# Kernel optimization log

Measured on AMD Instinct MI355X. Metric: run time of the kernel, lower is better.

## Reference

```python
import jax, jax.numpy as jnp
import numpy as np

D_MODEL = 1024
D_STATE = 128
D_CONV = 4
EXPAND = 2
HEADDIM = 64
NGROUPS = 1
CHUNK = 256
D_INNER = EXPAND * D_MODEL          # 2048
NHEADS = D_INNER // HEADDIM         # 32
D_IN_PROJ = 2 * D_INNER + 2 * NGROUPS * D_STATE + NHEADS  # 4384
CONV_DIM = D_INNER + 2 * NGROUPS * D_STATE                # 2304
BATCH, SEQLEN = 2, 2048


def rmsnorm(x, w, eps=1e-6):
    ms = jnp.mean(x * x, axis=-1, keepdims=True)
    return w * (x * jax.lax.rsqrt(ms + eps))


def layernorm(x, eps=1e-5):
    mu = jnp.mean(x, axis=-1, keepdims=True)
    var = jnp.mean((x - mu) ** 2, axis=-1, keepdims=True)
    return (x - mu) * jax.lax.rsqrt(var + eps)


def activation_quant(x):
    # int8-style fake quant with STE, scale differentiable (matches torch)
    amax = jnp.clip(jnp.max(jnp.abs(x), axis=-1, keepdims=True), 1e-5, None)
    scale = 127.0 / amax
    q = jnp.clip(jnp.round(x * scale), -128, 127)
    return (jax.lax.stop_gradient(q - x * scale) + x * scale) / scale


def weight_quant(w):
    # ternary {-1,0,1}; note: NOT rescaled by scale (matches the triton kernel)
    scale = jnp.clip(jnp.mean(jnp.abs(w)), 1e-5, None)
    wq = jnp.clip(jnp.round(w / scale), -1.0, 1.0)
    return w + jax.lax.stop_gradient(wq - w)  # STE: identity grad


def bitlinear(x, w):
    return activation_quant(layernorm(x)) @ weight_quant(w).T


def segsum(x):
    # x: [..., T] -> [..., T, T] lower-triangular cumulative segment sums
    T = x.shape[-1]
    cs = jnp.cumsum(x, axis=-1)
    ss = cs[..., :, None] - cs[..., None, :]
    mask = jnp.tril(jnp.ones((T, T), dtype=bool))
    return jnp.where(mask, ss, -jnp.inf)


def ssd(u, a, B, C, chunk):
    # u: b l h p (= x*dt); a: b l h (= A*dt); B, C: b l h n (per-head)
    b, l, h, p = u.shape
    n = B.shape[-1]
    c = l // chunk
    u = u.reshape(b, c, chunk, h, p)
    a = a.reshape(b, c, chunk, h).transpose(0, 3, 1, 2)   # b h c s
    B = B.reshape(b, c, chunk, h, n)
    C = C.reshape(b, c, chunk, h, n)
    a_cs = jnp.cumsum(a, axis=-1)                          # b h c s
    L = jnp.exp(segsum(a))                                 # b h c s s
    Y_diag = jnp.einsum('bclhn,bcshn,bhcls,bcshp->bclhp', C, B, L, u)
    decay_states = jnp.exp(a_cs[..., -1:] - a_cs)          # b h c s
    states = jnp.einsum('bclhn,bhcl,bclhp->bchpn', B, decay_states, u)
    a_chunk = jnp.pad(a_cs[..., -1], ((0, 0), (0, 0), (1, 0)))  # b h (c+1)
    decay_chunk = jnp.exp(segsum(a_chunk))                 # b h (c+1) (c+1)
    states = jnp.concatenate([jnp.zeros_like(states[:, :1]), states], axis=1)
    new_states = jnp.einsum('bhzc,bchpn->bzhpn', decay_chunk, states)
    prev_states = new_states[:, :-1]                       # state entering each chunk
    Y_off = jnp.einsum('bclhn,bchpn,bhcl->bclhp', C, prev_states, jnp.exp(a_cs))
    return (Y_diag + Y_off).reshape(b, l, h, p)


def setup_inputs() -> dict:
    key = jax.random.key(0)
    ks = jax.random.split(key, 6)
    hidden_states = jax.random.normal(ks[0], (BATCH, SEQLEN, D_MODEL), jnp.float32)
    in_proj_w = jax.random.normal(ks[1], (D_IN_PROJ, D_MODEL), jnp.float32) / np.sqrt(D_MODEL).astype(np.float32)
    out_proj_w = jax.random.normal(ks[2], (D_MODEL, D_INNER), jnp.float32) / np.sqrt(D_INNER).astype(np.float32)
    conv_w = jax.random.normal(ks[3], (CONV_DIM, D_CONV), jnp.float32) * 0.1
    conv_b = jnp.zeros((CONV_DIM,), jnp.float32)
    A_log = jnp.log(jnp.arange(1, NHEADS + 1, dtype=jnp.float32))
    Dp = jnp.ones((NHEADS,), jnp.float32)
    dt_min, dt_max, dt_floor = 1e-3, 1e-1, 1e-4
    inv_dt = jnp.exp(jax.random.uniform(ks[4], (NHEADS,)) * (np.log(dt_max) - np.log(dt_min)) + np.log(dt_min))
    inv_dt = jnp.clip(inv_dt, dt_floor, None)
    dt_bias = inv_dt + jnp.log(-jnp.expm1(-inv_dt))
    norm_w = jnp.ones((D_MODEL,), jnp.float32)
    out_norm_w = jnp.ones((D_INNER,), jnp.float32)
    return dict(hidden_states=hidden_states, norm_w=norm_w, in_proj_w=in_proj_w,
                conv_w=conv_w, conv_b=conv_b, A_log=A_log, Dp=Dp, dt_bias=dt_bias,
                out_norm_w=out_norm_w, out_proj_w=out_proj_w)


def reference(hidden_states, norm_w, in_proj_w, conv_w, conv_b, A_log, Dp, dt_bias, out_norm_w, out_proj_w):
    b, l, _ = hidden_states.shape
    h = rmsnorm(hidden_states, norm_w)
    zxbcdt = bitlinear(h, in_proj_w)                       # b l (2*d_inner + 2*g*n + h)
    z = zxbcdt[..., :D_INNER]
    xBC = zxbcdt[..., D_INNER:D_INNER + CONV_DIM]
    dt = zxbcdt[..., D_INNER + CONV_DIM:]                  # b l h
    # causal depthwise conv1d (kernel D_CONV) + silu
    xp = jnp.pad(xBC, ((0, 0), (D_CONV - 1, 0), (0, 0)))
    conv = sum(xp[:, k:k + l, :] * conv_w[:, k] for k in range(D_CONV)) + conv_b
    xBC = jax.nn.silu(conv)
    x = xBC[..., :D_INNER].reshape(b, l, NHEADS, HEADDIM)
    Bm = xBC[..., D_INNER:D_INNER + NGROUPS * D_STATE].reshape(b, l, NGROUPS, D_STATE)
    Cm = xBC[..., D_INNER + NGROUPS * D_STATE:].reshape(b, l, NGROUPS, D_STATE)
    hpg = NHEADS // NGROUPS
    Bh = jnp.repeat(Bm, hpg, axis=2)                       # b l h n
    Ch = jnp.repeat(Cm, hpg, axis=2)
    dt = jax.nn.softplus(dt + dt_bias)                     # dt_softplus=True
    A = -jnp.exp(A_log)
    y = ssd(x * dt[..., None], dt * A, Bh, Ch, CHUNK)      # b l h p
    y = y + x * Dp[None, None, :, None]                    # D skip
    y = y * jax.nn.silu(z).reshape(b, l, NHEADS, HEADDIM)  # z gate
    y = rmsnorm(y.reshape(b, l, D_INNER), out_norm_w)
    out = bitlinear(y, out_proj_w)
    return hidden_states + out
```

## Files before the change

### kernel.cpp

```cpp
#include <hip/hip_runtime.h>
#include <stdint.h>
#include <stddef.h>
#include <math.h>

#define TOKS 4096
#define DM   1024
#define DIP  4384
#define DI   2048
#define CVD  2304
#define NH   32
#define HD   64
#define DST  128
#define NCH  8
#define CHK  256

typedef int v4i  __attribute__((ext_vector_type(4)));
typedef int v16i __attribute__((ext_vector_type(16)));
typedef short s8v __attribute__((ext_vector_type(8)));
typedef float f16v __attribute__((ext_vector_type(16)));
typedef unsigned short ushort_t;

static const size_t OFF_ZX    = 0;
static const size_t OFF_SX    = OFF_ZX + (size_t)TOKS*DIP*4;
static const size_t OFF_ST    = OFF_SX + (size_t)TOKS*CVD*4;
static const size_t OFF_YG    = OFF_ST + (size_t)512*HD*DST*4;
static const size_t OFF_Q1    = OFF_YG + (size_t)TOKS*DI*4;
static const size_t OFF_Q2    = OFF_Q1 + (size_t)TOKS*DM;
static const size_t OFF_WQ1   = OFF_Q2 + (size_t)TOKS*DI;
static const size_t OFF_WQ2   = OFF_WQ1 + (size_t)DIP*DM;
static const size_t OFF_RS1   = OFF_WQ2 + (size_t)DM*DI;
static const size_t OFF_RS2   = OFF_RS1 + (size_t)TOKS*4;
static const size_t OFF_DT    = OFF_RS2 + (size_t)TOKS*4;
static const size_t OFF_ACS   = OFF_DT + (size_t)TOKS*NH*4;
static const size_t OFF_CSUM  = OFF_ACS + (size_t)512*CHK*8;
static const size_t OFF_PART  = OFF_CSUM + 512*8;
static const size_t OFF_WSC   = OFF_PART + 1024*8;
static const size_t OFF_BH    = OFF_WSC + 64;
static const size_t OFF_BL    = OFF_BH  + (size_t)TOKS*128*2;
static const size_t OFF_CHG   = OFF_BL  + (size_t)TOKS*128*2;
static const size_t OFF_CLG   = OFF_CHG + (size_t)TOKS*128*2;
static const size_t OFF_GRAM  = OFF_CLG + (size_t)TOKS*128*2;
static const size_t OFF_UTH   = OFF_GRAM + (size_t)16*256*256*4;
static const size_t OFF_UTL   = OFF_UTH + (size_t)512*64*256*2;
static const size_t OFF_PH    = OFF_UTL + (size_t)512*64*256*2;
static const size_t OFF_PL    = OFF_PH  + (size_t)512*64*128*2;

__device__ __forceinline__ ushort_t f2bf(float x) {
  union { float f; unsigned int u; } v; v.f = x;
  unsigned int r = v.u + 0x7FFFu + ((v.u >> 16) & 1u);
  return (ushort_t)(r >> 16);
}
__device__ __forceinline__ float bf2f(ushort_t h) {
  union { unsigned int u; float f; } v; v.u = ((unsigned int)h) << 16;
  return v.f;
}

__device__ __forceinline__ double bsumd(double v, double* sb) {
#pragma unroll
  for (int o = 32; o; o >>= 1) v += __shfl_down(v, o);
  int lane = threadIdx.x & 63, w = threadIdx.x >> 6;
  __syncthreads();
  if (lane == 0) sb[w] = v;
  __syncthreads();
  return sb[0] + sb[1] + sb[2] + sb[3];
}
__device__ __forceinline__ double bmaxd(double v, double* sb) {
#pragma unroll
  for (int o = 32; o; o >>= 1) v = fmax(v, __shfl_down(v, o));
  int lane = threadIdx.x & 63, w = threadIdx.x >> 6;
  __syncthreads();
  if (lane == 0) sb[w] = v;
  __syncthreads();
  return fmax(fmax(sb[0], sb[1]), fmax(sb[2], sb[3]));
}

__global__ void __launch_bounds__(256) k_absmean(const float* __restrict__ w, int n, double* __restrict__ part) {
  double s = 0.0;
  for (int i = blockIdx.x * 256 + threadIdx.x; i < n; i += 512 * 256) s += (double)fabsf(w[i]);
  __shared__ double sb[4];
  s = bsumd(s, sb);
  if (threadIdx.x == 0) part[blockIdx.x] = s;
}

__global__ void __launch_bounds__(256) k_wscale(const double* __restrict__ part, double* __restrict__ wsc, int n1, int n2) {
  __shared__ double sb[4];
  double s = part[threadIdx.x] + part[threadIdx.x + 256];
  double t1 = bsumd(s, sb);
  __syncthreads();
  s = part[512 + threadIdx.x] + part[512 + threadIdx.x + 256];
  double t2 = bsumd(s, sb);
  if (threadIdx.x == 0) {
    wsc[0] = fmax(t1 / (double)n1, 1e-5);
    wsc[1] = fmax(t2 / (double)n2, 1e-5);
  }
}

__global__ void __launch_bounds__(256) k_tern(const float* __restrict__ w, int n, const double* __restrict__ wsc, int which, int8_t* __restrict__ out) {
  int i = blockIdx.x * 256 + threadIdx.x;
  if (i < n) {
    double sc = wsc[which];
    double q = fmin(fmax(rint((double)w[i] / sc), -1.0), 1.0);
    out[i] = (int8_t)q;
  }
}

template <int D>
__global__ void __launch_bounds__(256) k_normquant(const float* __restrict__ in, const float* __restrict__ w,
                                                   int8_t* __restrict__ q, float* __restrict__ rs) {
  constexpr int E = D / 256;
  int t = blockIdx.x, tid = threadIdx.x;
  const float* row = in + (size_t)t * D;
  __shared__ double sb[4];
  double x[E];
  double ss = 0.0;
#pragma unroll
  for (int i = 0; i < E; i++) { x[i] = (double)row[tid + 256 * i]; ss += x[i] * x[i]; }
  ss = bsumd(ss, sb);
  double rr = 1.0 / sqrt(ss / (double)D + 1e-6);
  double s1 = 0.0;
#pragma unroll
  for (int i = 0; i < E; i++) { x[i] = (double)w[tid + 256 * i] * (x[i] * rr); s1 += x[i]; }
  s1 = bsumd(s1, sb);
  double mu = s1 / (double)D;
  double s2 = 0.0;
#pragma unroll
  for (int i = 0; i < E; i++) { double d = x[i] - mu; s2 += d * d; }
  s2 = bsumd(s2, sb);
  double rv = 1.0 / sqrt(s2 / (double)D + 1e-5);
  double am = 0.0;
#pragma unroll
  for (int i = 0; i < E; i++) { x[i] = (x[i] - mu) * rv; am = fmax(am, fabs(x[i])); }
  am = bmaxd(am, sb);
  am = fmax(am, 1e-5);
  double sc = 127.0 / am;
#pragma unroll
  for (int i = 0; i < E; i++) {
    double qq = fmin(fmax(rint(x[i] * sc), -128.0), 127.0);
    q[(size_t)t * D + tid + 256 * i] = (int8_t)qq;
  }
  if (tid == 0) rs[t] = (float)(am / 127.0);
}

__global__ void __launch_bounds__(256, 3) k_gemm_mfma(const int8_t* __restrict__ A, const int8_t* __restrict__ W,
                                                      const float* __restrict__ rs, const float* __restrict__ addend,
                                                      float* __restrict__ out, int M, int N, int K) {
  __shared__ int8_t Al[128 * 80];
  __shared__ int8_t Bl[128 * 80];
  int m0 = blockIdx.x * 128, n0 = blockIdx.y * 128;
  int t = threadIdx.x;
  int w = t >> 6, lane = t & 63;
  int wm = w >> 1, wn = w & 1;
  int l31 = lane & 31, lh = lane >> 5;

  v16i acc[2][2] = {};

  for (int k0 = 0; k0 < K; k0 += 64) {
    __syncthreads();
#pragma unroll
    for (int it = 0; it < 2; ++it) {
      int c = t + 256 * it;
      int row = c >> 2, kc = (c & 3) * 16;
      int4 av = *(const int4*)(A + (size_t)(m0 + row) * K + k0 + kc);
      *(int4*)(Al + row * 80 + kc) = av;
      int4 bv;
      if (n0 + row < N) bv = *(const int4*)(W + (size_t)(n0 + row) * K + k0 + kc);
      else { bv.x = bv.y = bv.z = bv.w = 0; }
      *(int4*)(Bl + row * 80 + kc) = bv;
    }
    __syncthreads();
#pragma unroll
    for (int ks = 0; ks < 2; ++ks) {
      v4i af[2], bf[2];
#pragma unroll
      for (int tm = 0; tm < 2; ++tm)
        af[tm] = *(const v4i*)(Al + (wm * 64 + tm * 32 + l31) * 80 + ks * 32 + lh * 16);
#pragma unroll
      for (int tn = 0; tn < 2; ++tn)
        bf[tn] = *(const v4i*)(Bl + (wn * 64 + tn * 32 + l31) * 80 + ks * 32 + lh * 16);
#pragma unroll
      for (int tm = 0; tm < 2; ++tm)
#pragma unroll
        for (int tn = 0; tn < 2; ++tn)
          acc[tm][tn] = __builtin_amdgcn_mfma_i32_32x32x32_i8(af[tm], bf[tn], acc[tm][tn], 0, 0, 0);
    }
  }

#pragma unroll
  for (int tm = 0; tm < 2; ++tm)
#pragma unroll
    for (int tn = 0; tn < 2; ++tn) {
      int n = n0 + wn * 64 + tn * 32 + l31;
      if (n < N) {
#pragma unroll
        for (int r = 0; r < 16; ++r) {
          int mrel = (r & 3) + 8 * (r >> 2) + 4 * lh;
          int m = m0 + wm * 64 + tm * 32 + mrel;
          float v = rs[m] * (float)acc[tm][tn][r];
          if (addend) v += addend[(size_t)m * N + n];
          out[(size_t)m * N + n] = v;
        }
      }
    }
}

__global__ void __launch_bounds__(256) k_conv(const float* __restrict__ zx, const float* __restrict__ cw,
                                              const float* __restrict__ cb, float* __restrict__ sx) {
  int c = blockIdx.x * 256 + threadIdx.x;
  int t = blockIdx.y;
  int b = t >> 11, l = t & 2047;
  float acc = cb[c];
#pragma unroll
  for (int k = 0; k < 4; k++) {
    int li = l - 3 + k;
    if (li >= 0) acc = fmaf(zx[(size_t)(b * 2048 + li) * DIP + DI + c], cw[c * 4 + k], acc);
  }
  sx[(size_t)t * CVD + c] = acc / (1.f + expf(-acc));
}

__global__ void __launch_bounds__(256) k_splitbc(const float* __restrict__ sx,
                                                 ushort_t* __restrict__ bh, ushort_t* __restrict__ bl,
                                                 ushort_t* __restrict__ ch, ushort_t* __restrict__ cl) {
  int idx = blockIdx.x * 256 + threadIdx.x;
  int tok = idx >> 6, c4 = (idx & 63) * 4;
  float4 v = *(const float4*)(sx + (size_t)tok * CVD + DI + c4);
  float f[4] = {v.x, v.y, v.z, v.w};
  ushort_t hh[4], ll[4];
#pragma unroll
  for (int j = 0; j < 4; j++) { hh[j] = f2bf(f[j]); ll[j] = f2bf(f[j] - bf2f(hh[j])); }
  uint2 hv, lv;
  hv.x = (unsigned)hh[0] | ((unsigned)hh[1] << 16); hv.y = (unsigned)hh[2] | ((unsigned)hh[3] << 16);
  lv.x = (unsigned)ll[0] | ((unsigned)ll[1] << 16); lv.y = (unsigned)ll[2] | ((unsigned)ll[3] << 16);
  if (c4 < 128) {
    *(uint2*)(bh + (size_t)tok * 128 + c4) = hv;
    *(uint2*)(bl + (size_t)tok * 128 + c4) = lv;
  } else {
    *(uint2*)(ch + (size_t)tok * 128 + c4 - 128) = hv;
    *(uint2*)(cl + (size_t)tok * 128 + c4 - 128) = lv;
  }
}

__global__ void __launch_bounds__(256) k_dt(const float* __restrict__ zx, const float* __restrict__ dt_bias,
                                            float* __restrict__ dtv) {
  int idx = blockIdx.x * 256 + threadIdx.x;
  int t = idx >> 5, h = idx & 31;
  float x = zx[(size_t)t * DIP + (DI + CVD) + h] + dt_bias[h];
  dtv[idx] = fmaxf(x, 0.f) + log1pf(expf(-fabsf(x)));
}

__global__ void __launch_bounds__(256) k_cumsum(const float* __restrict__ dtv, const float* __restrict__ A_log,
                                                double* __restrict__ acs, double* __restrict__ csum) {
  int bid = blockIdx.x;
  int h = bid & 31, bc = bid >> 5;
  int s = threadIdx.x;
  int tok = bc * 256 + s;
  double negA = -exp((double)A_log[h]);
  double a = (double)dtv[tok * 32 + h] * negA;
  __shared__ double buf[256];
  buf[s] = a;
  __syncthreads();
  for (int o = 1; o < 256; o <<= 1) {
    double add = (s >= o) ? buf[s - o] : 0.0;
    __syncthreads();
    buf[s] += add;
    __syncthreads();
  }
  acs[(size_t)bid * 256 + s] = buf[s];
  if (s == 255) csum[bid] = buf[s];
}

__global__ void __launch_bounds__(256) k_gram(const ushort_t* __restrict__ bhg, const ushort_t* __restrict__ blg,
                                              const ushort_t* __restrict__ chg, const ushort_t* __restrict__ clg,
                                              float* __restrict__ gram) {
  int blk = blockIdx.x;
  int bc = blk >> 3, lt = blk & 7;
  int t = threadIdx.x;
  int w = t >> 6, lane = t & 63;
  int l31 = lane & 31, lhf = lane >> 5;
  __shared__ float Gl[4][32 * 36];

  s8v ch[8], cl[8];
  size_t tokA = (size_t)(bc * 256 + lt * 32 + l31) * 128;
#pragma unroll
  for (int ks = 0; ks < 8; ++ks) {
    ch[ks] = *(const s8v*)(chg + tokA + ks * 16 + lhf * 8);
    cl[ks] = *(const s8v*)(clg + tokA + ks * 16 + lhf * 8);
  }
  for (int st = w; st <= lt; st += 4) {
    size_t tokB = (size_t)(bc * 256 + st * 32 + l31) * 128;
    f16v acc = {};
#pragma unroll
    for (int ks = 0; ks < 8; ++ks) {
      s8v bh = *(const s8v*)(bhg + tokB + ks * 16 + lhf * 8);
      s8v bl = *(const s8v*)(blg + tokB + ks * 16 + lhf * 8);
      acc = __builtin_amdgcn_mfma_f32_32x32x16_bf16(ch[ks], bh, acc, 0, 0, 0);
      acc = __builtin_amdgcn_mfma_f32_32x32x16_bf16(ch[ks], bl, acc, 0, 0, 0);
      acc = __builtin_amdgcn_mfma_f32_32x32x16_bf16(cl[ks], bh, acc, 0, 0, 0);
    }
#pragma unroll
    for (int rr = 0; rr < 16; ++rr) {
      int lrow = (rr & 3) + 8 * (rr >> 2) + 4 * lhf;
      Gl[w][lrow * 36 + l31] = acc[rr];
    }
    int lr = lane >> 1, c0 = (lane & 1) * 16;
    float* gdst = gram + ((size_t)bc * 256 + lt * 32 + lr) * 256 + st * 32 + c0;
#pragma unroll
    for (int i = 0; i < 4; ++i)
      *(float4*)(gdst + i * 4) = *(const float4*)(&Gl[w][lr * 36 + c0 + i * 4]);
  }
}

__global__ void __launch_bounds__(256) k_prepuT(const float* __restrict__ sx, const float* __restrict__ dtv,
                                                ushort_t* __restrict__ uth, ushort_t* __restrict__ utl) {
  int r = blockIdx.x;
  int h = r & 31, bc = r >> 5;
  int t = threadIdx.x;
  __shared__ float Xs[64 * 68];
  __shared__ float dts[64];
  for (int slab = 0; slab < 4; ++slab) {
    int s0 = slab * 64;
    if (slab) __syncthreads();
    if (t < 64) dts[t] = dtv[(size_t)(bc * 256 + s0 + t) * 32 + h];
    {
      int s = t >> 2, pg = (t & 3) * 16;
      const float* xr = sx + (size_t)(bc * 256 + s0 + s) * CVD + h * 64 + pg;
      float* dst = &Xs[s * 68 + pg];
#pragma unroll
      for (int i = 0; i < 4; ++i)
        *(float4*)(dst + i * 4) = *(const float4*)(xr + i * 4);
    }
    __syncthreads();
    {
      int p = t >> 2, sg = (t & 3) * 16;
      union { int4 q[2]; ushort_t e[16]; } H, L;
#pragma unroll
      for (int j = 0; j < 16; ++j) {
        float f = Xs[(sg + j) * 68 + p] * dts[sg + j];
        ushort_t hh = f2bf(f);
        H.e[j] = hh;
        L.e[j] = f2bf(f - bf2f(hh));
      }
      size_t base = ((size_t)r * 64 + p) * 256 + s0 + sg;
      *(int4*)(uth + base) = H.q[0];
      *(int4*)(uth + base + 8) = H.q[1];
      *(int4*)(utl + base) = L.q[0];
      *(int4*)(utl + base + 8) = L.q[1];
    }
  }
}

__global__ void __launch_bounds__(256, 4) k_states2(const float* __restrict__ sx, const float* __restrict__ dtv,
                                                    const double* __restrict__ acs, const double* __restrict__ csum,
                                                    float* __restrict__ states) {
  int r = blockIdx.x;
  int h = r & 31, bc = r >> 5;
  int t = threadIdx.x, tx = t & 15, ty = t >> 4;
  __shared__ float du[64 * 68];
  double last = csum[r];
  float acc[4][8] = {};
  for (int s0 = 0; s0 < 256; s0 += 64) {
    __syncthreads();
    {
      int s = t >> 2, pg = (t & 3) * 16;
      int tok = bc * 256 + s0 + s;
      float w = expf((float)(last - acs[(size_t)r * 256 + s0 + s])) * dtv[(size_t)tok * 32 + h];
      const float* xr = sx + (size_t)tok * CVD + h * 64 + pg;
      float* dst = &du[s * 68 + pg];
#pragma unroll
      for (int i = 0; i < 4; i++) {
        float4 v = *(const float4*)(xr + i * 4);
        v.x *= w; v.y *= w; v.z *= w; v.w *= w;
        *(float4*)(dst + i * 4) = v;
      }
    }
    __syncthreads();
#pragma unroll 4
    for (int s = 0; s < 64; s++) {
      int tok = bc * 256 + s0 + s;
      const float* br = sx + (size_t)tok * CVD + DI + ty * 8;
      float4 b0 = *(const float4*)(br);
      float4 b1 = *(const float4*)(br + 4);
      float4 d4 = *(const float4*)(&du[s * 68 + tx * 4]);
      float dd[4] = {d4.x, d4.y, d4.z, d4.w};
      float bv[8] = {b0.x, b0.y, b0.z, b0.w, b1.x, b1.y, b1.z, b1.w};
#pragma unroll
      for (int i = 0; i < 4; i++)
#pragma unroll
        for (int j = 0; j < 8; j++) acc[i][j] = fmaf(dd[i], bv[j], acc[i][j]);
    }
  }
  size_t base = (size_t)r * (HD * DST);
#pragma unroll
  for (int i = 0; i < 4; i++) {
    float4 v0, v1;
    v0.x = acc[i][0]; v0.y = acc[i][1]; v0.z = acc[i][2]; v0.w = acc[i][3];
    v1.x = acc[i][4]; v1.y = acc[i][5]; v1.z = acc[i][6]; v1.w = acc[i][7];
    *(float4*)(states + base + (size_t)(tx * 4 + i) * DST + ty * 8) = v0;
    *(float4*)(states + base + (size_t)(tx * 4 + i) * DST + ty * 8 + 4) = v1;
  }
}

__global__ void __launch_bounds__(256) k_chunkscan(float* __restrict__ states, const double* __restrict__ csum,
                                                   ushort_t* __restrict__ ph, ushort_t* __restrict__ pl) {
  int idx = blockIdx.x * 256 + threadIdx.x;
  int n = idx & 127, p = (idx >> 7) & 63, h = (idx >> 13) & 31, b = idx >> 18;
  float Nv = 0.f;
  for (int c = 0; c < 8; c++) {
    int bid = (b * 8 + c) * 32 + h;
    size_t addr = (size_t)bid * (HD * DST) + p * DST + n;
    float s = states[addr];
    states[addr] = Nv;
    ushort_t hh = f2bf(Nv);
    ph[addr] = hh;
    pl[addr] = f2bf(Nv - bf2f(hh));
    Nv = Nv * expf((float)csum[bid]) + s;
  }
}

__global__ void __launch_bounds__(64) k_y7(const float* __restrict__ sx, const double* __restrict__ acs,
                                           const ushort_t* __restrict__ chg, const ushort_t* __restrict__ clg,
                                           const ushort_t* __restrict__ prevh, const ushort_t* __restrict__ prevl,
                                           const float* __restrict__ gram,
                                           const ushort_t* __restrict__ uth, const ushort_t* __restrict__ utl,
                                           const float* __restrict__ zx, const float* __restrict__ Dp,
                                           float* __restrict__ yg) {
  int myid = (blockIdx.x & 7) * 512 + (blockIdx.x >> 3);
  int r = myid >> 3, lt = myid & 7;
  int h = r & 31, bc = r >> 5;
  int lane = threadIdx.x;
  int l31 = lane & 31, lhf = lane >> 5;
  int lw = lt * 32;
  int lg = lw + l31;
  const double* acsr = acs + (size_t)r * 256;
  double a_l = acsr[lg];

  f16v Yacc[2] = {};
  {
    size_t ca = (size_t)(bc * 256 + lg) * 128;
#pragma unroll
    for (int ks = 0; ks < 8; ++ks) {
      s8v ch = *(const s8v*)(chg + ca + ks * 16 + lhf * 8);
      s8v cl = *(const s8v*)(clg + ca + ks * 16 + lhf * 8);
#pragma unroll
      for (int pt = 0; pt < 2; ++pt) {
        size_t pa = ((size_t)r * 64 + pt * 32 + l31) * 128 + ks * 16 + lhf * 8;
        s8v ph = *(const s8v*)(prevh + pa);
        s8v pl = *(const s8v*)(prevl + pa);
        Yacc[pt] = __builtin_amdgcn_mfma_f32_32x32x16_bf16(ch, ph, Yacc[pt], 0, 0, 0);
        Yacc[pt] = __builtin_amdgcn_mfma_f32_32x32x16_bf16(ch, pl, Yacc[pt], 0, 0, 0);
        Yacc[pt] = __builtin_amdgcn_mfma_f32_32x32x16_bf16(cl, ph, Yacc[pt], 0, 0, 0);
      }
    }
  }
#pragma unroll
  for (int rr = 0; rr < 16; ++rr) {
    int lrow = (rr & 3) + 8 * (rr >> 2) + 4 * lhf;
    float el = expf((float)acsr[lw + lrow]);
    Yacc[0][rr] *= el;
    Yacc[1][rr] *= el;
  }

  for (int st = 0; st <= lt; ++st) {
    int s0 = st * 32;
    const float* gp = gram + (size_t)(bc * 256 + lg) * 256 + s0;
#pragma unroll
    for (int ks2 = 0; ks2 < 2; ++ks2) {
      int kb = ks2 * 16 + lhf * 8;
      float4 g0 = *(const float4*)(gp + kb);
      float4 g1 = *(const float4*)(gp + kb + 4);
      float gv[8] = {g0.x, g0.y, g0.z, g0.w, g1.x, g1.y, g1.z, g1.w};
      union { s8v v; ushort_t e[8]; } AH, AL;
#pragma unroll
      for (int j = 0; j < 8; ++j) {
        int s = s0 + kb + j;
        float v = 0.f;
        if (s <= lg) v = expf((float)(a_l - acsr[s])) * gv[j];
        ushort_t hh = f2bf(v);
        AH.e[j] = hh;
        AL.e[j] = f2bf(v - bf2f(hh));
      }
#pragma unroll
      for (int pt = 0; pt < 2; ++pt) {
        size_t ub = ((size_t)r * 64 + pt * 32 + l31) * 256 + s0 + kb;
        s8v uh = *(const s8v*)(uth + ub);
        s8v ul = *(const s8v*)(utl + ub);
        Yacc[pt] = __builtin_amdgcn_mfma_f32_32x32x16_bf16(AH.v, uh, Yacc[pt], 0, 0, 0);
        Yacc[pt] = __builtin_amdgcn_mfma_f32_32x32x16_bf16(AH.v, ul, Yacc[pt], 0, 0, 0);
        Yacc[pt] = __builtin_amdgcn_mfma_f32_32x32x16_bf16(AL.v, uh, Yacc[pt], 0, 0, 0);
      }
    }
  }

  float dph = Dp[h];
#pragma unroll
  for (int pt = 0; pt < 2; ++pt) {
    int p = pt * 32 + l31;
#pragma unroll
    for (int rr = 0; rr < 16; ++rr) {
      int lrow = (rr & 3) + 8 * (rr >> 2) + 4 * lhf;
      size_t tok = (size_t)(bc * 256 + lw + lrow);
      float xv = sx[tok * CVD + h * 64 + p];
      float zv = zx[tok * DIP + h * 64 + p];
      float y = (Yacc[pt][rr] + xv * dph) * (zv / (1.f + expf(-zv)));
      yg[tok * DI + h * 64 + p] = y;
    }
  }
}

extern "C" void kernel_launch(void* const* d_in, const int* in_sizes, int n_in,
                              void* d_out, int out_size, void* d_ws, size_t ws_size,
                              hipStream_t stream) {
  const float* hidden   = (const float*)d_in[0];
  const float* norm_w   = (const float*)d_in[1];
  const float* in_proj  = (const float*)d_in[2];
  const float* conv_w   = (const float*)d_in[3];
  const float* conv_b   = (const float*)d_in[4];
  const float* A_log    = (const float*)d_in[5];
  const float* Dp       = (const float*)d_in[6];
  const float* dt_bias  = (const float*)d_in[7];
  const float* out_norm = (const float*)d_in[8];
  const float* out_proj = (const float*)d_in[9];
  float* out = (float*)d_out;

  char* ws = (char*)d_ws;
  float*  zx    = (float*)(ws + OFF_ZX);
  float*  sx    = (float*)(ws + OFF_SX);
  float*  st    = (float*)(ws + OFF_ST);
  float*  yg    = (float*)(ws + OFF_YG);
  int8_t* q1    = (int8_t*)(ws + OFF_Q1);
  int8_t* q2    = (int8_t*)(ws + OFF_Q2);
  int8_t* wq1   = (int8_t*)(ws + OFF_WQ1);
  int8_t* wq2   = (int8_t*)(ws + OFF_WQ2);
  float*  rs1   = (float*)(ws + OFF_RS1);
  float*  rs2   = (float*)(ws + OFF_RS2);
  float*  dtv   = (float*)(ws + OFF_DT);
  double* acs   = (double*)(ws + OFF_ACS);
  double* csum  = (double*)(ws + OFF_CSUM);
  double* part  = (double*)(ws + OFF_PART);
  double* wsc   = (double*)(ws + OFF_WSC);
  ushort_t* bhg = (ushort_t*)(ws + OFF_BH);
  ushort_t* blg = (ushort_t*)(ws + OFF_BL);
  ushort_t* chg = (ushort_t*)(ws + OFF_CHG);
  ushort_t* clg = (ushort_t*)(ws + OFF_CLG);
  float*  gram  = (float*)(ws + OFF_GRAM);
  ushort_t* uth = (ushort_t*)(ws + OFF_UTH);
  ushort_t* utl = (ushort_t*)(ws + OFF_UTL);
  ushort_t* pvh = (ushort_t*)(ws + OFF_PH);
  ushort_t* pvl = (ushort_t*)(ws + OFF_PL);

  const int n1 = DIP * DM, n2 = DM * DI;

  hipLaunchKernelGGL(k_absmean, dim3(512), dim3(256), 0, stream, in_proj, n1, part);
  hipLaunchKernelGGL(k_absmean, dim3(512), dim3(256), 0, stream, out_proj, n2, part + 512);
  hipLaunchKernelGGL(k_wscale, dim3(1), dim3(256), 0, stream, part, wsc, n1, n2);
  hipLaunchKernelGGL(k_tern, dim3((n1 + 255) / 256), dim3(256), 0, stream, in_proj, n1, wsc, 0, wq1);
  hipLaunchKernelGGL(k_tern, dim3((n2 + 255) / 256), dim3(256), 0, stream, out_proj, n2, wsc, 1, wq2);
  hipLaunchKernelGGL(k_normquant<DM>, dim3(TOKS), dim3(256), 0, stream, hidden, norm_w, q1, rs1);
  hipLaunchKernelGGL(k_gemm_mfma, dim3(TOKS / 128, (DIP + 127) / 128), dim3(256), 0, stream,
                     q1, wq1, rs1, (const float*)nullptr, zx, TOKS, DIP, DM);
  hipLaunchKernelGGL(k_conv, dim3(CVD / 256, TOKS), dim3(256), 0, stream, zx, conv_w, conv_b, sx);
  hipLaunchKernelGGL(k_splitbc, dim3(TOKS * 64 / 256), dim3(256), 0, stream, sx, bhg, blg, chg, clg);
  hipLaunchKernelGGL(k_dt, dim3(TOKS * NH / 256), dim3(256), 0, stream, zx, dt_bias, dtv);
  hipLaunchKernelGGL(k_cumsum, dim3(512), dim3(256), 0, stream, dtv, A_log, acs, csum);
  hipLaunchKernelGGL(k_gram, dim3(128), dim3(256), 0, stream, bhg, blg, chg, clg, gram);
  hipLaunchKernelGGL(k_prepuT, dim3(512), dim3(256), 0, stream, sx, dtv, uth, utl);
  hipLaunchKernelGGL(k_states2, dim3(512), dim3(256), 0, stream, sx, dtv, acs, csum, st);
  hipLaunchKernelGGL(k_chunkscan, dim3(2 * NH * HD * DST / 256), dim3(256), 0, stream, st, csum, pvh, pvl);
  hipLaunchKernelGGL(k_y7, dim3(4096), dim3(64), 0, stream, sx, acs, chg, clg, pvh, pvl, gram, uth, utl, zx, Dp, yg);
  hipLaunchKernelGGL(k_normquant<DI>, dim3(TOKS), dim3(256), 0, stream, yg, out_norm, q2, rs2);
  hipLaunchKernelGGL(k_gemm_mfma, dim3(TOKS / 128, DM / 128), dim3(256), 0, stream,
                     q2, wq2, rs2, hidden, out, TOKS, DM, DI);
  (void)in_sizes; (void)n_in; (void)out_size; (void)ws_size;
}
```

Measured before the change: 419.2 us.

## Fuse norm reductions, fold BC split into conv, software-pipeline y kernel

Result: no change. 422.0 us (+0.7%).

```diff
diff --git a/kernel.cpp b/kernel.cpp
--- a/kernel.cpp
+++ b/kernel.cpp
@@ -73,6 +73,21 @@
   __syncthreads();
   return fmax(fmax(sb[0], sb[1]), fmax(sb[2], sb[3]));
 }
+__device__ __forceinline__ void bsum3d(double& a, double& b, double& c, double* sb) {
+#pragma unroll
+  for (int o = 32; o; o >>= 1) {
+    a += __shfl_down(a, o);
+    b += __shfl_down(b, o);
+    c += __shfl_down(c, o);
+  }
+  int lane = threadIdx.x & 63, w = threadIdx.x >> 6;
+  __syncthreads();
+  if (lane == 0) { sb[w * 3 + 0] = a; sb[w * 3 + 1] = b; sb[w * 3 + 2] = c; }
+  __syncthreads();
+  a = sb[0] + sb[3] + sb[6] + sb[9];
+  b = sb[1] + sb[4] + sb[7] + sb[10];
+  c = sb[2] + sb[5] + sb[8] + sb[11];
+}
 
 __global__ void __launch_bounds__(256) k_absmean(const float* __restrict__ w, int n, double* __restrict__ part) {
   double s = 0.0;
@@ -110,32 +125,33 @@
   constexpr int E = D / 256;
   int t = blockIdx.x, tid = threadIdx.x;
   const float* row = in + (size_t)t * D;
-  __shared__ double sb[4];
-  double x[E];
-  double ss = 0.0;
-#pragma unroll
-  for (int i = 0; i < E; i++) { x[i] = (double)row[tid + 256 * i]; ss += x[i] * x[i]; }
-  ss = bsumd(ss, sb);
-  double rr = 1.0 / sqrt(ss / (double)D + 1e-6);
-  double s1 = 0.0;
-#pragma unroll
-  for (int i = 0; i < E; i++) { x[i] = (double)w[tid + 256 * i] * (x[i] * rr); s1 += x[i]; }
-  s1 = bsumd(s1, sb);
-  double mu = s1 / (double)D;
-  double s2 = 0.0;
-#pragma unroll
-  for (int i = 0; i < E; i++) { double d = x[i] - mu; s2 += d * d; }
-  s2 = bsumd(s2, sb);
-  double rv = 1.0 / sqrt(s2 / (double)D + 1e-5);
-  double am = 0.0;
-#pragma unroll
-  for (int i = 0; i < E; i++) { x[i] = (x[i] - mu) * rv; am = fmax(am, fabs(x[i])); }
-  am = bmaxd(am, sb);
-  am = fmax(am, 1e-5);
+  __shared__ double sb[12];
+  double y[E];
+  double s0 = 0.0, s1 = 0.0, s2 = 0.0;
+#pragma unroll
+  for (int i = 0; i < E; i++) {
+    double xv = (double)row[tid + 256 * i];
+    double wv = (double)w[tid + 256 * i];
+    s0 += xv * xv;
+    double yy = wv * xv;
+    y[i] = yy;
+    s1 += yy;
+    s2 += yy * yy;
+  }
+  bsum3d(s0, s1, s2, sb);
+  double rr = 1.0 / sqrt(s0 / (double)D + 1e-6);
+  double mu = rr * (s1 / (double)D);
+  double var = rr * rr * (s2 / (double)D) - mu * mu;
+  double rv = 1.0 / sqrt(var + 1e-5);
+  double M = 0.0;
+#pragma unroll
+  for (int i = 0; i < E; i++) { y[i] = y[i] * rr - mu; M = fmax(M, fabs(y[i])); }
+  M = bmaxd(M, sb);
+  double am = fmax(M * rv, 1e-5);
   double sc = 127.0 / am;
 #pragma unroll
   for (int i = 0; i < E; i++) {
-    double qq = fmin(fmax(rint(x[i] * sc), -128.0), 127.0);
+    double qq = fmin(fmax(rint(y[i] * rv * sc), -128.0), 127.0);
     q[(size_t)t * D + tid + 256 * i] = (int8_t)qq;
   }
   if (tid == 0) rs[t] = (float)(am / 127.0);
@@ -204,7 +220,9 @@
 }
 
 __global__ void __launch_bounds__(256) k_conv(const float* __restrict__ zx, const float* __restrict__ cw,
-                                              const float* __restrict__ cb, float* __restrict__ sx) {
+                                              const float* __restrict__ cb, float* __restrict__ sx,
+                                              ushort_t* __restrict__ bh, ushort_t* __restrict__ bl,
+                                              ushort_t* __restrict__ ch, ushort_t* __restrict__ cl) {
   int c = blockIdx.x * 256 + threadIdx.x;
   int t = blockIdx.y;
   int b = t >> 11, l = t & 2047;
@@ -214,28 +232,19 @@
     int li = l - 3 + k;
     if (li >= 0) acc = fmaf(zx[(size_t)(b * 2048 + li) * DIP + DI + c], cw[c * 4 + k], acc);
   }
-  sx[(size_t)t * CVD + c] = acc / (1.f + expf(-acc));
-}
-
-__global__ void __launch_bounds__(256) k_splitbc(const float* __restrict__ sx,
-                                                 ushort_t* __restrict__ bh, ushort_t* __restrict__ bl,
-                                                 ushort_t* __restrict__ ch, ushort_t* __restrict__ cl) {
-  int idx = blockIdx.x * 256 + threadIdx.x;
-  int tok = idx >> 6, c4 = (idx & 63) * 4;
-  float4 v = *(const float4*)(sx + (size_t)tok * CVD + DI + c4);
-  float f[4] = {v.x, v.y, v.z, v.w};
-  ushort_t hh[4], ll[4];
-#pragma unroll
-  for (int j = 0; j < 4; j++) { hh[j] = f2bf(f[j]); ll[j] = f2bf(f[j] - bf2f(hh[j])); }
-  uint2 hv, lv;
-  hv.x = (unsigned)hh[0] | ((unsigned)hh[1] << 16); hv.y = (unsigned)hh[2] | ((unsigned)hh[3] << 16);
-  lv.x = (unsigned)ll[0] | ((unsigned)ll[1] << 16); lv.y = (unsigned)ll[2] | ((unsigned)ll[3] << 16);
-  if (c4 < 128) {
-    *(uint2*)(bh + (size_t)tok * 128 + c4) = hv;
-    *(uint2*)(bl + (size_t)tok * 128 + c4) = lv;
-  } else {
-    *(uint2*)(ch + (size_t)tok * 128 + c4 - 128) = hv;
-    *(uint2*)(cl + (size_t)tok * 128 + c4 - 128) = lv;
+  float val = acc / (1.f + expf(-acc));
+  sx[(size_t)t * CVD + c] = val;
+  if (c >= DI) {
+    int idx = c - DI;
+    ushort_t hh = f2bf(val);
+    ushort_t ll = f2bf(val - bf2f(hh));
+    if (idx < 128) {
+      bh[(size_t)t * 128 + idx] = hh;
+      bl[(size_t)t * 128 + idx] = ll;
+    } else {
+      ch[(size_t)t * 128 + idx - 128] = hh;
+      cl[(size_t)t * 128 + idx - 128] = ll;
+    }
   }
 }
 
@@ -416,7 +425,7 @@
   }
 }
 
-__global__ void __launch_bounds__(64) k_y7(const float* __restrict__ sx, const double* __restrict__ acs,
+__global__ void __launch_bounds__(64) k_y8(const float* __restrict__ sx, const double* __restrict__ acs,
                                            const ushort_t* __restrict__ chg, const ushort_t* __restrict__ clg,
                                            const ushort_t* __restrict__ prevh, const ushort_t* __restrict__ prevl,
                                            const float* __restrict__ gram,
@@ -459,33 +468,83 @@
     Yacc[1][rr] *= el;
   }
 
+  const float* gbase = gram + (size_t)(bc * 256 + lg) * 256;
+  size_t ub0 = ((size_t)r * 64 + l31) * 256;
+  size_t ub1 = ((size_t)r * 64 + 32 + l31) * 256;
+
+  s8v AH[2], AL[2], UH[4], UL[4];
+  {
+#pragma unroll
+    for (int k2 = 0; k2 < 2; ++k2) {
+      int sb = k2 * 16 + lhf * 8;
+      float4 g0 = *(const float4*)(gbase + sb);
+      float4 g1 = *(const float4*)(gbase + sb + 4);
+      float gv[8] = {g0.x, g0.y, g0.z, g0.w, g1.x, g1.y, g1.z, g1.w};
+      union { s8v v; ushort_t e[8]; } H, L;
+#pragma unroll
+      for (int j = 0; j < 8; ++j) {
+        float v = 0.f;
+        if (sb + j <= lg) v = expf((float)(a_l - acsr[sb + j])) * gv[j];
+        ushort_t hh = f2bf(v);
+        H.e[j] = hh;
+        L.e[j] = f2bf(v - bf2f(hh));
+      }
+      AH[k2] = H.v; AL[k2] = L.v;
+      UH[k2 * 2 + 0] = *(const s8v*)(uth + ub0 + sb);
+      UH[k2 * 2 + 1] = *(const s8v*)(uth + ub1 + sb);
+      UL[k2 * 2 + 0] = *(const s8v*)(utl + ub0 + sb);
+      UL[k2 * 2 + 1] = *(const s8v*)(utl + ub1 + sb);
+    }
+  }
+
   for (int st = 0; st <= lt; ++st) {
-    int s0 = st * 32;
-    const float* gp = gram + (size_t)(bc * 256 + lg) * 256 + s0;
-#pragma unroll
-    for (int ks2 = 0; ks2 < 2; ++ks2) {
-      int kb = ks2 * 16 + lhf * 8;
-      float4 g0 = *(const float4*)(gp + kb);
-      float4 g1 = *(const float4*)(gp + kb + 4);
-      float gv[8] = {g0.x, g0.y, g0.z, g0.w, g1.x, g1.y, g1.z, g1.w};
-      union { s8v v; ushort_t e[8]; } AH, AL;
-#pragma unroll
-      for (int j = 0; j < 8; ++j) {
-        int s = s0 + kb + j;
-        float v = 0.f;
-        if (s <= lg) v = expf((float)(a_l - acsr[s])) * gv[j];
-        ushort_t hh = f2bf(v);
-        AH.e[j] = hh;
-        AL.e[j] = f2bf(v - bf2f(hh));
-      }
+    float4 ng0[2], ng1[2];
+    s8v nUH[4], nUL[4];
+    bool more = (st < lt);
+    int s1 = (st + 1) * 32;
+    if (more) {
+#pragma unroll
+      for (int k2 = 0; k2 < 2; ++k2) {
+        int sb = s1 + k2 * 16 + lhf * 8;
+        ng0[k2] = *(const float4*)(gbase + sb);
+        ng1[k2] = *(const float4*)(gbase + sb + 4);
+        nUH[k2 * 2 + 0] = *(const s8v*)(uth + ub0 + sb);
+        nUH[k2 * 2 + 1] = *(const s8v*)(uth + ub1 + sb);
+        nUL[k2 * 2 + 0] = *(const s8v*)(utl + ub0 + sb);
+        nUL[k2 * 2 + 1] = *(const s8v*)(utl + ub1 + sb);
+      }
+    }
+    __builtin_amdgcn_s_setprio(1);
+#pragma unroll
+    for (int k2 = 0; k2 < 2; ++k2) {
 #pragma unroll
       for (int pt = 0; pt < 2; ++pt) {
-        size_t ub = ((size_t)r * 64 + pt * 32 + l31) * 256 + s0 + kb;
-        s8v uh = *(const s8v*)(uth + ub);
-        s8v ul = *(const s8v*)(utl + ub);
-        Yacc[pt] = __builtin_amdgcn_mfma_f32_32x32x16_bf16(AH.v, uh, Yacc[pt], 0, 0, 0);
-        Yacc[pt] = __builtin_amdgcn_mfma_f32_32x32x16_bf16(AH.v, ul, Yacc[pt], 0, 0, 0);
-        Yacc[pt] = __builtin_amdgcn_mfma_f32_32x32x16_bf16(AL.v, uh, Yacc[pt], 0, 0, 0);
+        Yacc[pt] = __builtin_amdgcn_mfma_f32_32x32x16_bf16(AH[k2], UH[k2 * 2 + pt], Yacc[pt], 0, 0, 0);
+        Yacc[pt] = __builtin_amdgcn_mfma_f32_32x32x16_bf16(AH[k2], UL[k2 * 2 + pt], Yacc[pt], 0, 0, 0);
+        Yacc[pt] = __builtin_amdgcn_mfma_f32_32x32x16_bf16(AL[k2], UH[k2 * 2 + pt], Yacc[pt], 0, 0, 0);
+      }
+    }
+    __builtin_amdgcn_s_setprio(0);
+    if (more) {
+#pragma unroll
+      for (int k2 = 0; k2 < 2; ++k2) {
+        int sb = s1 + k2 * 16 + lhf * 8;
+        float gv[8] = {ng0[k2].x, ng0[k2].y, ng0[k2].z, ng0[k2].w,
+                       ng1[k2].x, ng1[k2].y, ng1[k2].z, ng1[k2].w};
+        union { s8v v; ushort_t e[8]; } H, L;
+#pragma unroll
+        for (int j = 0; j < 8; ++j) {
+          float v = 0.f;
+          if (sb + j <= lg) v = expf((float)(a_l - acsr[sb + j])) * gv[j];
+          ushort_t hh = f2bf(v);
+          H.e[j] = hh;
+          L.e[j] = f2bf(v - bf2f(hh));
+        }
+        AH[k2] = H.v; AL[k2] = L.v;
+        UH[k2 * 2 + 0] = nUH[k2 * 2 + 0];
+        UH[k2 * 2 + 1] = nUH[k2 * 2 + 1];
+        UL[k2 * 2 + 0] = nUL[k2 * 2 + 0];
+        UL[k2 * 2 + 1] = nUL[k2 * 2 + 1];
       }
     }
   }
@@ -557,15 +616,15 @@
   hipLaunchKernelGGL(k_normquant<DM>, dim3(TOKS), dim3(256), 0, stream, hidden, norm_w, q1, rs1);
   hipLaunchKernelGGL(k_gemm_mfma, dim3(TOKS / 128, (DIP + 127) / 128), dim3(256), 0, stream,
                      q1, wq1, rs1, (const float*)nullptr, zx, TOKS, DIP, DM);
-  hipLaunchKernelGGL(k_conv, dim3(CVD / 256, TOKS), dim3(256), 0, stream, zx, conv_w, conv_b, sx);
-  hipLaunchKernelGGL(k_splitbc, dim3(TOKS * 64 / 256), dim3(256), 0, stream, sx, bhg, blg, chg, clg);
+  hipLaunchKernelGGL(k_conv, dim3(CVD / 256, TOKS), dim3(256), 0, stream, zx, conv_w, conv_b, sx,
+                     bhg, blg, chg, clg);
   hipLaunchKernelGGL(k_dt, dim3(TOKS * NH / 256), dim3(256), 0, stream, zx, dt_bias, dtv);
   hipLaunchKernelGGL(k_cumsum, dim3(512), dim3(256), 0, stream, dtv, A_log, acs, csum);
   hipLaunchKernelGGL(k_gram, dim3(128), dim3(256), 0, stream, bhg, blg, chg, clg, gram);
   hipLaunchKernelGGL(k_prepuT, dim3(512), dim3(256), 0, stream, sx, dtv, uth, utl);
   hipLaunchKernelGGL(k_states2, dim3(512), dim3(256), 0, stream, sx, dtv, acs, csum, st);
   hipLaunchKernelGGL(k_chunkscan, dim3(2 * NH * HD * DST / 256), dim3(256), 0, stream, st, csum, pvh, pvl);
-  hipLaunchKernelGGL(k_y7, dim3(4096), dim3(64), 0, stream, sx, acs, chg, clg, pvh, pvl, gram, uth, utl, zx, Dp, yg);
+  hipLaunchKernelGGL(k_y8, dim3(4096), dim3(64), 0, stream, sx, acs, chg, clg, pvh, pvl, gram, uth, utl, zx, Dp, yg);
   hipLaunchKernelGGL(k_normquant<DI>, dim3(TOKS), dim3(256), 0, stream, yg, out_norm, q2, rs2);
   hipLaunchKernelGGL(k_gemm_mfma, dim3(TOKS / 128, DM / 128), dim3(256), 0, stream,
                      q2, wq2, rs2, hidden, out, TOKS, DM, DI);
```
